# Kernel tuning notes

Measured on AMD Instinct MI355X. Metric: run time of the kernel, lower is better.

Reference implementation:

```python
import jax, jax.numpy as jnp
import numpy as np


def setup_inputs() -> dict:
    key = jax.random.key(0)
    ks = jax.random.split(key, 7)
    B, S, D, F, E = 4, 2048, 1024, 4096, 8
    scale = 0.02
    return {
        "x": jax.random.normal(ks[0], (B, S, D), dtype=jnp.float32),
        "gate_w": jax.random.normal(ks[1], (D, E), dtype=jnp.float32) * scale,
        "gate_b": jnp.zeros((E,), dtype=jnp.float32),
        "w1": jax.random.normal(ks[2], (E, D, F), dtype=jnp.float32) * scale,
        "b1": jnp.zeros((E, F), dtype=jnp.float32),
        "w2": jax.random.normal(ks[3], (E, F, D), dtype=jnp.float32) * scale,
        "b2": jnp.zeros((E, D), dtype=jnp.float32),
        "top_k": 2,
    }


def reference(x, gate_w, gate_b, w1, b1, w2, b2, top_k):
    B, S, D = x.shape
    E = w1.shape[0]
    xf = x.reshape(-1, D)                      # [T, D], T = B*S
    T = xf.shape[0]

    # Router: top-k logits, softmax over the selected k (as in torch code)
    logits = xf @ gate_w + gate_b              # [T, E]
    rw, sel = jax.lax.top_k(logits, top_k)     # [T, k], [T, k]
    w = jax.nn.softmax(rw, axis=-1)            # [T, k]

    # Dense combine weights: combine[t, e] = sum_k w[t,k] * (sel[t,k]==e)
    combine = jnp.zeros((T, E), dtype=xf.dtype)
    combine = combine.at[jnp.arange(T)[:, None], sel].add(w)

    # Loop over small fixed expert count; each expert FFN on all tokens,
    # weighted by combine (zero for unrouted tokens). Dropout p honored as 0 (eval).
    out = jnp.zeros_like(xf)
    for e in range(E):
        h = jax.nn.gelu(xf @ w1[e] + b1[e], approximate=False)  # torch F.gelu = exact
        out = out + combine[:, e:e + 1] * (h @ w2[e] + b2[e])
    return out.reshape(B, S, D)
```

## Files before the change

kernel.cpp:

```cpp
#include <hip/hip_runtime.h>
#include <math.h>

#define T_TOK 8192
#define DDIM  1024
#define FDIM  4096
#define NEXP  8
#define MAXTILES 136

typedef __attribute__((ext_vector_type(8))) short short8;
typedef __attribute__((ext_vector_type(4))) float f32x4;
typedef unsigned short u16;
typedef unsigned int   u32;

typedef const __attribute__((address_space(1))) u32* gp_t;
typedef       __attribute__((address_space(3))) u32* lp_t;

__device__ __forceinline__ void gload16(const void* g, void* l) {
  __builtin_amdgcn_global_load_lds((gp_t)g, (lp_t)l, 16, 0, 0);
}

__device__ __forceinline__ u16 f2bf(float f) {
  u32 u = __float_as_uint(f);
  u = u + 0x7FFFu + ((u >> 16) & 1u);
  return (u16)(u >> 16);
}

__device__ __forceinline__ float gelu_exact(float v) {
  return 0.5f * v * (1.0f + erff(v * 0.70710678118654752440f));
}

__device__ __forceinline__ int xcd_swz(int orig, int nwg) {
  int xcd = orig & 7;
  int q = nwg >> 3, r = nwg & 7;
  int base = (xcd < r) ? xcd * (q + 1) : r * (q + 1) + (xcd - r) * q;
  return base + (orig >> 3);
}

__global__ __launch_bounds__(256) void router_kernel(
    const float* __restrict__ x, const float* __restrict__ gw,
    const float* __restrict__ gb, u16* __restrict__ xb,
    int* __restrict__ counts, int* __restrict__ sel, float* __restrict__ wts)
{
  const int t    = blockIdx.x * 4 + (threadIdx.x >> 6);
  const int lane = threadIdx.x & 63;
  const float* xr = x + (size_t)t * DDIM;
  u16* xbr = xb + (size_t)t * DDIM;
  float lg[NEXP];
  #pragma unroll
  for (int e = 0; e < NEXP; e++) lg[e] = 0.f;
  #pragma unroll
  for (int i = 0; i < 4; i++) {
    int d0 = i * 256 + lane * 4;
    float4 v = *(const float4*)(xr + d0);
    ushort4 o;
    o.x = f2bf(v.x); o.y = f2bf(v.y); o.z = f2bf(v.z); o.w = f2bf(v.w);
    *(ushort4*)(xbr + d0) = o;
    const float* g = gw + (size_t)d0 * NEXP;
    #pragma unroll
    for (int e = 0; e < NEXP; e++)
      lg[e] += v.x * g[e] + v.y * g[NEXP + e] + v.z * g[2 * NEXP + e] + v.w * g[3 * NEXP + e];
  }
  #pragma unroll
  for (int off = 32; off > 0; off >>= 1) {
    #pragma unroll
    for (int e = 0; e < NEXP; e++) lg[e] += __shfl_down(lg[e], off);
  }
  if (lane == 0) {
    float v0 = -1e30f, v1 = -1e30f; int s0 = 0, s1 = 0;
    #pragma unroll
    for (int e = 0; e < NEXP; e++) {
      float v = lg[e] + gb[e];
      if (v > v0) { v1 = v0; s1 = s0; v0 = v; s0 = e; }
      else if (v > v1) { v1 = v; s1 = e; }
    }
    float a  = expf(v1 - v0);
    float w0 = 1.f / (1.f + a);
    sel[t * 2] = s0; sel[t * 2 + 1] = s1;
    wts[t * 2] = w0; wts[t * 2 + 1] = 1.f - w0;
    atomicAdd(&counts[s0], 1); atomicAdd(&counts[s1], 1);
  }
}

__global__ void scan_kernel(const int* __restrict__ counts,
                            int* __restrict__ offsets, int* __restrict__ pos,
                            int* __restrict__ map_e, int* __restrict__ map_r,
                            int* __restrict__ nT)
{
  if (threadIdx.x == 0) {
    int run = 0, nt = 0;
    for (int e = 0; e < NEXP; e++) {
      offsets[e] = run; pos[e] = run;
      int c = counts[e];
      int ntile = (c + 127) >> 7;
      for (int i = 0; i < ntile; i++) { map_e[nt] = e; map_r[nt] = i * 128; nt++; }
      run += c;
    }
    nT[0] = nt;
  }
}

__global__ __launch_bounds__(256) void slot_assign_kernel(
    const int* __restrict__ sel, const float* __restrict__ wts,
    int* __restrict__ pos, int* __restrict__ slot_token,
    float* __restrict__ slot_weight, int* __restrict__ token_slot)
{
  const int t = blockIdx.x * 256 + threadIdx.x;
  #pragma unroll
  for (int k = 0; k < 2; k++) {
    int e = sel[t * 2 + k];
    int p = atomicAdd(&pos[e], 1);
    slot_token[p] = t; slot_weight[p] = wts[t * 2 + k];
    token_slot[t * 2 + k] = p;
  }
}

__global__ __launch_bounds__(256) void wtrans_kernel(
    const float* __restrict__ in, u16* __restrict__ out, int M, int N)
{
  const int e = blockIdx.z;
  in  += (size_t)e * M * N;
  out += (size_t)e * M * N;
  const int c0 = blockIdx.x * 64;
  const int r0 = blockIdx.y * 64;
  __shared__ float tile[64][65];
  const int tid = threadIdx.x;
  const int tr = tid >> 4;
  const int tc = (tid & 15) * 4;
  #pragma unroll
  for (int p = 0; p < 4; p++) {
    int r = p * 16 + tr;
    float4 v = *(const float4*)(in + (size_t)(r0 + r) * N + (c0 + tc));
    tile[r][tc] = v.x; tile[r][tc + 1] = v.y; tile[r][tc + 2] = v.z; tile[r][tc + 3] = v.w;
  }
  __syncthreads();
  #pragma unroll
  for (int p = 0; p < 4; p++) {
    int oc = p * 16 + tr;
    ushort4 o;
    o.x = f2bf(tile[tc][oc]);     o.y = f2bf(tile[tc + 1][oc]);
    o.z = f2bf(tile[tc + 2][oc]); o.w = f2bf(tile[tc + 3][oc]);
    *(ushort4*)(out + (size_t)(c0 + oc) * M + (r0 + tc)) = o;
  }
}

__global__ __launch_bounds__(256) void gemm1_kernel(
    const u16* __restrict__ XB, const u16* __restrict__ W1T,
    const float* __restrict__ B1,
    const int* __restrict__ counts, const int* __restrict__ offsets,
    const int* __restrict__ slot_token,
    const int* __restrict__ map_e, const int* __restrict__ map_r,
    const int* __restrict__ nT, u16* __restrict__ H)
{
  const int gid   = xcd_swz(blockIdx.x, gridDim.x);
  const int n_idx = gid / MAXTILES;
  const int t_idx = gid - n_idx * MAXTILES;
  if (t_idx >= nT[0]) return;
  const int e    = map_e[t_idx];
  const int row0 = map_r[t_idx];
  const int cnt  = counts[e];
  const int off  = offsets[e];
  const int n0   = n_idx * 128;

  __shared__ __align__(16) u16 As[128 * 32];
  __shared__ __align__(16) u16 Bs[128 * 32];

  const int tid = threadIdx.x, wave = tid >> 6, lane = tid & 63;
  const int ca = wave * 64 + lane;
  const int rA0 = ca >> 2, sl0 = ca & 3;

  int t0 = slot_token[off + row0 + rA0];      if ((u32)t0 >= T_TOK) t0 = 0;
  int t1 = slot_token[off + row0 + rA0 + 64]; if ((u32)t1 >= T_TOK) t1 = 0;
  const char* gA0 = (const char*)XB + (((size_t)t0 * DDIM) + sl0 * 8) * 2;
  const char* gA1 = (const char*)XB + (((size_t)t1 * DDIM) + sl0 * 8) * 2;
  char* lA0 = (char*)As + wave * 1024;
  char* lA1 = (char*)As + 4096 + wave * 1024;

  const char* gB0 = (const char*)W1T + (((size_t)(e * FDIM + n0 + rA0)) * DDIM + sl0 * 8) * 2;
  const char* gB1 = (const char*)W1T + (((size_t)(e * FDIM + n0 + rA0 + 64)) * DDIM + sl0 * 8) * 2;
  char* lB0 = (char*)Bs + wave * 1024;
  char* lB1 = (char*)Bs + 4096 + wave * 1024;

  f32x4 acc[4][4] = {};
  const int wr = wave >> 1, wc = wave & 1;
  const int lr = lane & 15, lk = (lane >> 4) * 8;

  for (int k0 = 0; k0 < DDIM; k0 += 32) {
    __syncthreads();
    gload16(gA0 + k0 * 2, lA0);
    gload16(gA1 + k0 * 2, lA1);
    gload16(gB0 + k0 * 2, lB0);
    gload16(gB1 + k0 * 2, lB1);
    __syncthreads();

    short8 a[4], b[4];
    #pragma unroll
    for (int m = 0; m < 4; m++)
      a[m] = *(const short8*)&As[(wr * 64 + m * 16 + lr) * 32 + lk];
    #pragma unroll
    for (int n = 0; n < 4; n++)
      b[n] = *(const short8*)&Bs[(wc * 64 + n * 16 + lr) * 32 + lk];
    #pragma unroll
    for (int m = 0; m < 4; m++)
      #pragma unroll
      for (int n = 0; n < 4; n++)
        acc[m][n] = __builtin_amdgcn_mfma_f32_16x16x32_bf16(a[m], b[n], acc[m][n], 0, 0, 0);
  }

  #pragma unroll
  for (int nn = 0; nn < 4; nn++) {
    int col = n0 + wc * 64 + nn * 16 + lr;
    float b1v = B1[e * FDIM + col];
    #pragma unroll
    for (int m = 0; m < 4; m++) {
      int rbase = wr * 64 + m * 16 + (lane >> 4) * 4;
      #pragma unroll
      for (int j = 0; j < 4; j++) {
        int r = rbase + j;
        if (row0 + r < cnt) {
          float v = acc[m][nn][j] + b1v;
          H[(size_t)(off + row0 + r) * FDIM + col] = f2bf(gelu_exact(v));
        }
      }
    }
  }
}

__global__ __launch_bounds__(256) void gemm2_kernel(
    const u16* __restrict__ H, const u16* __restrict__ W2T,
    const float* __restrict__ B2,
    const int* __restrict__ counts, const int* __restrict__ offsets,
    const int* __restrict__ map_e, const int* __restrict__ map_r,
    const int* __restrict__ nT, float* __restrict__ Y)
{
  const int gid   = xcd_swz(blockIdx.x, gridDim.x);
  const int n_idx = gid / MAXTILES;
  const int t_idx = gid - n_idx * MAXTILES;
  if (t_idx >= nT[0]) return;
  const int e    = map_e[t_idx];
  const int row0 = map_r[t_idx];
  const int cnt  = counts[e];
  const int off  = offsets[e];
  const int n0   = n_idx * 128;

  __shared__ __align__(16) u16 As[128 * 32];
  __shared__ __align__(16) u16 Bs[128 * 32];

  const int tid = threadIdx.x, wave = tid >> 6, lane = tid & 63;
  const int ca = wave * 64 + lane;
  const int rA0 = ca >> 2, sl0 = ca & 3;

  const char* gA0 = (const char*)H + ((size_t)(off + row0 + rA0) * FDIM + sl0 * 8) * 2;
  const char* gA1 = (const char*)H + ((size_t)(off + row0 + rA0 + 64) * FDIM + sl0 * 8) * 2;
  char* lA0 = (char*)As + wave * 1024;
  char* lA1 = (char*)As + 4096 + wave * 1024;

  const char* gB0 = (const char*)W2T + ((size_t)(e * DDIM + n0 + rA0) * FDIM + sl0 * 8) * 2;
  const char* gB1 = (const char*)W2T + ((size_t)(e * DDIM + n0 + rA0 + 64) * FDIM + sl0 * 8) * 2;
  char* lB0 = (char*)Bs + wave * 1024;
  char* lB1 = (char*)Bs + 4096 + wave * 1024;

  f32x4 acc[4][4] = {};
  const int wr = wave >> 1, wc = wave & 1;
  const int lr = lane & 15, lk = (lane >> 4) * 8;

  for (int k0 = 0; k0 < FDIM; k0 += 32) {
    __syncthreads();
    gload16(gA0 + k0 * 2, lA0);
    gload16(gA1 + k0 * 2, lA1);
    gload16(gB0 + k0 * 2, lB0);
    gload16(gB1 + k0 * 2, lB1);
    __syncthreads();

    short8 a[4], b[4];
    #pragma unroll
    for (int m = 0; m < 4; m++)
      a[m] = *(const short8*)&As[(wr * 64 + m * 16 + lr) * 32 + lk];
    #pragma unroll
    for (int n = 0; n < 4; n++)
      b[n] = *(const short8*)&Bs[(wc * 64 + n * 16 + lr) * 32 + lk];
    #pragma unroll
    for (int m = 0; m < 4; m++)
      #pragma unroll
      for (int n = 0; n < 4; n++)
        acc[m][n] = __builtin_amdgcn_mfma_f32_16x16x32_bf16(a[m], b[n], acc[m][n], 0, 0, 0);
  }

  #pragma unroll
  for (int m = 0; m < 4; m++) {
    int rbase = wr * 64 + m * 16 + (lane >> 4) * 4;
    #pragma unroll
    for (int j = 0; j < 4; j++) {
      int r = rbase + j;
      if (row0 + r >= cnt) continue;
      size_t s = (size_t)(off + row0 + r);
      #pragma unroll
      for (int nn = 0; nn < 4; nn++) {
        int col = n0 + wc * 64 + nn * 16 + lr;
        Y[s * DDIM + col] = acc[m][nn][j] + B2[e * DDIM + col];
      }
    }
  }
}

__global__ __launch_bounds__(256) void combine_kernel(
    const float* __restrict__ Y, const int* __restrict__ token_slot,
    const float* __restrict__ wts, float* __restrict__ out)
{
  size_t gid = (size_t)blockIdx.x * 256 + threadIdx.x;
  int t = (int)(gid >> 8);
  int c = (int)(gid & 255) * 4;
  int s0 = token_slot[t * 2], s1 = token_slot[t * 2 + 1];
  float w0 = wts[t * 2], w1 = wts[t * 2 + 1];
  float4 y0 = *(const float4*)&Y[(size_t)s0 * DDIM + c];
  float4 y1 = *(const float4*)&Y[(size_t)s1 * DDIM + c];
  float4 o;
  o.x = w0 * y0.x + w1 * y1.x; o.y = w0 * y0.y + w1 * y1.y;
  o.z = w0 * y0.z + w1 * y1.z; o.w = w0 * y0.w + w1 * y1.w;
  *(float4*)&out[(size_t)t * DDIM + c] = o;
}

extern "C" void kernel_launch(void* const* d_in, const int* in_sizes, int n_in,
                              void* d_out, int out_size, void* d_ws, size_t ws_size,
                              hipStream_t stream)
{
  (void)in_sizes; (void)n_in; (void)out_size; (void)ws_size;
  const float* x  = (const float*)d_in[0];
  const float* gw = (const float*)d_in[1];
  const float* gb = (const float*)d_in[2];
  const float* w1 = (const float*)d_in[3];
  const float* b1 = (const float*)d_in[4];
  const float* w2 = (const float*)d_in[5];
  const float* b2 = (const float*)d_in[6];

  char* ws = (char*)d_ws;
  int*   counts = (int*)(ws + 0);
  int*   posp   = (int*)(ws + 64);
  int*   offp   = (int*)(ws + 128);
  int*   nT     = (int*)(ws + 192);
  int*   map_e  = (int*)(ws + 256);
  int*   map_r  = (int*)(ws + 1024);

  size_t p = 2048;
  int*   sel   = (int*)(ws + p);   p += (size_t)T_TOK * 2 * 4;
  float* wts   = (float*)(ws + p); p += (size_t)T_TOK * 2 * 4;
  int*   stok  = (int*)(ws + p);  p += (size_t)(2 * T_TOK + 256) * 4;
  float* swgt  = (float*)(ws + p); p += (size_t)(2 * T_TOK + 256) * 4;
  int*   tslot = (int*)(ws + p);  p += (size_t)T_TOK * 2 * 4;
  p = (p + 1048575) & ~(size_t)1048575;
  u16*   xb    = (u16*)(ws + p);  p += (size_t)T_TOK * DDIM * 2;
  u16*   w1t   = (u16*)(ws + p);  p += (size_t)NEXP * DDIM * FDIM * 2;
  u16*   w2t   = (u16*)(ws + p);  p += (size_t)NEXP * DDIM * FDIM * 2;
  u16*   Hbuf  = (u16*)(ws + p);  p += (size_t)(2 * T_TOK + 128) * FDIM * 2;
  float* Ybuf  = (float*)(ws + p);

  hipMemsetAsync(ws, 0, 256, stream);
  router_kernel<<<T_TOK / 4, 256, 0, stream>>>(x, gw, gb, xb, counts, sel, wts);
  scan_kernel<<<1, 64, 0, stream>>>(counts, offp, posp, map_e, map_r, nT);
  slot_assign_kernel<<<T_TOK / 256, 256, 0, stream>>>(sel, wts, posp, stok, swgt, tslot);
  wtrans_kernel<<<dim3(FDIM / 64, DDIM / 64, NEXP), 256, 0, stream>>>(w1, w1t, DDIM, FDIM);
  wtrans_kernel<<<dim3(DDIM / 64, FDIM / 64, NEXP), 256, 0, stream>>>(w2, w2t, FDIM, DDIM);

  gemm1_kernel<<<(FDIM / 128) * MAXTILES, 256, 0, stream>>>(
      xb, w1t, b1, counts, offp, stok, map_e, map_r, nT, Hbuf);
  gemm2_kernel<<<(DDIM / 128) * MAXTILES, 256, 0, stream>>>(
      Hbuf, w2t, b2, counts, offp, map_e, map_r, nT, Ybuf);

  combine_kernel<<<(T_TOK * DDIM / 4) / 256, 256, 0, stream>>>(Ybuf, tslot, wts, (float*)d_out);
}
```

Baseline: 923.0 us.

## Double-buffer GEMM LDS tiles, fuse combine via atomics, widen weight transpose

Both expert GEMMs now double-buffer their LDS tiles, so the next K-slice's global-to-LDS load is issued before the MFMAs on the current slice, with one barrier per iteration instead of two. The combine kernel and the Y buffer are removed: gemm2 scales its output by the routing weight and atomically adds it into a zeroed output, saving a full fp32 intermediate write and re-read. The weight transpose uses 128-row tiles and writes 16-byte bf16 vectors. In exchange, the atomics make the fp32 summation order non-deterministic, and the larger LDS footprint may lower occupancy.

```diff
diff --git a/kernel.cpp b/kernel.cpp
--- a/kernel.cpp
+++ b/kernel.cpp
@@ -102,7 +102,7 @@
 __global__ __launch_bounds__(256) void slot_assign_kernel(
     const int* __restrict__ sel, const float* __restrict__ wts,
     int* __restrict__ pos, int* __restrict__ slot_token,
-    float* __restrict__ slot_weight, int* __restrict__ token_slot)
+    float* __restrict__ slot_weight)
 {
   const int t = blockIdx.x * 256 + threadIdx.x;
   #pragma unroll
@@ -110,7 +110,6 @@
     int e = sel[t * 2 + k];
     int p = atomicAdd(&pos[e], 1);
     slot_token[p] = t; slot_weight[p] = wts[t * 2 + k];
-    token_slot[t * 2 + k] = p;
   }
 }
 
@@ -120,26 +119,28 @@
   const int e = blockIdx.z;
   in  += (size_t)e * M * N;
   out += (size_t)e * M * N;
+  const int r0 = blockIdx.y * 128;
   const int c0 = blockIdx.x * 64;
-  const int r0 = blockIdx.y * 64;
-  __shared__ float tile[64][65];
+  __shared__ float tile[128][65];
   const int tid = threadIdx.x;
-  const int tr = tid >> 4;
-  const int tc = (tid & 15) * 4;
+  const int lr = tid >> 4;
+  const int lc = (tid & 15) * 4;
+  #pragma unroll
+  for (int p = 0; p < 8; p++) {
+    int r = p * 16 + lr;
+    float4 v = *(const float4*)(in + (size_t)(r0 + r) * N + (c0 + lc));
+    tile[r][lc] = v.x; tile[r][lc + 1] = v.y; tile[r][lc + 2] = v.z; tile[r][lc + 3] = v.w;
+  }
+  __syncthreads();
+  const int oc = tid >> 4;
+  const int om = (tid & 15) * 8;
   #pragma unroll
   for (int p = 0; p < 4; p++) {
-    int r = p * 16 + tr;
-    float4 v = *(const float4*)(in + (size_t)(r0 + r) * N + (c0 + tc));
-    tile[r][tc] = v.x; tile[r][tc + 1] = v.y; tile[r][tc + 2] = v.z; tile[r][tc + 3] = v.w;
-  }
-  __syncthreads();
-  #pragma unroll
-  for (int p = 0; p < 4; p++) {
-    int oc = p * 16 + tr;
-    ushort4 o;
-    o.x = f2bf(tile[tc][oc]);     o.y = f2bf(tile[tc + 1][oc]);
-    o.z = f2bf(tile[tc + 2][oc]); o.w = f2bf(tile[tc + 3][oc]);
-    *(ushort4*)(out + (size_t)(c0 + oc) * M + (r0 + tc)) = o;
+    int c = p * 16 + oc;
+    short8 o;
+    #pragma unroll
+    for (int j = 0; j < 8; j++) o[j] = (short)f2bf(tile[om + j][c]);
+    *(short8*)(out + (size_t)(c0 + c) * M + (r0 + om)) = o;
   }
 }
 
@@ -161,8 +162,8 @@
   const int off  = offsets[e];
   const int n0   = n_idx * 128;
 
-  __shared__ __align__(16) u16 As[128 * 32];
-  __shared__ __align__(16) u16 Bs[128 * 32];
+  __shared__ __align__(16) u16 As[2][128 * 32];
+  __shared__ __align__(16) u16 Bs[2][128 * 32];
 
   const int tid = threadIdx.x, wave = tid >> 6, lane = tid & 63;
   const int ca = wave * 64 + lane;
@@ -172,38 +173,45 @@
   int t1 = slot_token[off + row0 + rA0 + 64]; if ((u32)t1 >= T_TOK) t1 = 0;
   const char* gA0 = (const char*)XB + (((size_t)t0 * DDIM) + sl0 * 8) * 2;
   const char* gA1 = (const char*)XB + (((size_t)t1 * DDIM) + sl0 * 8) * 2;
-  char* lA0 = (char*)As + wave * 1024;
-  char* lA1 = (char*)As + 4096 + wave * 1024;
-
   const char* gB0 = (const char*)W1T + (((size_t)(e * FDIM + n0 + rA0)) * DDIM + sl0 * 8) * 2;
   const char* gB1 = (const char*)W1T + (((size_t)(e * FDIM + n0 + rA0 + 64)) * DDIM + sl0 * 8) * 2;
-  char* lB0 = (char*)Bs + wave * 1024;
-  char* lB1 = (char*)Bs + 4096 + wave * 1024;
+
+  char* baseA = (char*)As;
+  char* baseB = (char*)Bs;
+  auto stage = [&](int buf, int k0) {
+    char* a = baseA + buf * 8192 + wave * 1024;
+    char* b = baseB + buf * 8192 + wave * 1024;
+    gload16(gA0 + (size_t)k0 * 2, a);
+    gload16(gA1 + (size_t)k0 * 2, a + 4096);
+    gload16(gB0 + (size_t)k0 * 2, b);
+    gload16(gB1 + (size_t)k0 * 2, b + 4096);
+  };
 
   f32x4 acc[4][4] = {};
   const int wr = wave >> 1, wc = wave & 1;
   const int lr = lane & 15, lk = (lane >> 4) * 8;
 
-  for (int k0 = 0; k0 < DDIM; k0 += 32) {
-    __syncthreads();
-    gload16(gA0 + k0 * 2, lA0);
-    gload16(gA1 + k0 * 2, lA1);
-    gload16(gB0 + k0 * 2, lB0);
-    gload16(gB1 + k0 * 2, lB1);
-    __syncthreads();
-
+  stage(0, 0);
+  __syncthreads();
+  int cur = 0;
+  for (int t = 0; t < DDIM / 32; t++) {
+    if (t + 1 < DDIM / 32) stage(cur ^ 1, (t + 1) * 32);
+    const u16* Ab = As[cur];
+    const u16* Bb = Bs[cur];
     short8 a[4], b[4];
     #pragma unroll
     for (int m = 0; m < 4; m++)
-      a[m] = *(const short8*)&As[(wr * 64 + m * 16 + lr) * 32 + lk];
+      a[m] = *(const short8*)&Ab[(wr * 64 + m * 16 + lr) * 32 + lk];
     #pragma unroll
     for (int n = 0; n < 4; n++)
-      b[n] = *(const short8*)&Bs[(wc * 64 + n * 16 + lr) * 32 + lk];
+      b[n] = *(const short8*)&Bb[(wc * 64 + n * 16 + lr) * 32 + lk];
     #pragma unroll
     for (int m = 0; m < 4; m++)
       #pragma unroll
       for (int n = 0; n < 4; n++)
         acc[m][n] = __builtin_amdgcn_mfma_f32_16x16x32_bf16(a[m], b[n], acc[m][n], 0, 0, 0);
+    __syncthreads();
+    cur ^= 1;
   }
 
   #pragma unroll
@@ -229,8 +237,9 @@
     const u16* __restrict__ H, const u16* __restrict__ W2T,
     const float* __restrict__ B2,
     const int* __restrict__ counts, const int* __restrict__ offsets,
+    const int* __restrict__ slot_token, const float* __restrict__ slot_weight,
     const int* __restrict__ map_e, const int* __restrict__ map_r,
-    const int* __restrict__ nT, float* __restrict__ Y)
+    const int* __restrict__ nT, float* __restrict__ out)
 {
   const int gid   = xcd_swz(blockIdx.x, gridDim.x);
   const int n_idx = gid / MAXTILES;
@@ -242,8 +251,8 @@
   const int off  = offsets[e];
   const int n0   = n_idx * 128;
 
-  __shared__ __align__(16) u16 As[128 * 32];
-  __shared__ __align__(16) u16 Bs[128 * 32];
+  __shared__ __align__(16) u16 As[2][128 * 32];
+  __shared__ __align__(16) u16 Bs[2][128 * 32];
 
   const int tid = threadIdx.x, wave = tid >> 6, lane = tid & 63;
   const int ca = wave * 64 + lane;
@@ -251,38 +260,45 @@
 
   const char* gA0 = (const char*)H + ((size_t)(off + row0 + rA0) * FDIM + sl0 * 8) * 2;
   const char* gA1 = (const char*)H + ((size_t)(off + row0 + rA0 + 64) * FDIM + sl0 * 8) * 2;
-  char* lA0 = (char*)As + wave * 1024;
-  char* lA1 = (char*)As + 4096 + wave * 1024;
-
   const char* gB0 = (const char*)W2T + ((size_t)(e * DDIM + n0 + rA0) * FDIM + sl0 * 8) * 2;
   const char* gB1 = (const char*)W2T + ((size_t)(e * DDIM + n0 + rA0 + 64) * FDIM + sl0 * 8) * 2;
-  char* lB0 = (char*)Bs + wave * 1024;
-  char* lB1 = (char*)Bs + 4096 + wave * 1024;
+
+  char* baseA = (char*)As;
+  char* baseB = (char*)Bs;
+  auto stage = [&](int buf, int k0) {
+    char* a = baseA + buf * 8192 + wave * 1024;
+    char* b = baseB + buf * 8192 + wave * 1024;
+    gload16(gA0 + (size_t)k0 * 2, a);
+    gload16(gA1 + (size_t)k0 * 2, a + 4096);
+    gload16(gB0 + (size_t)k0 * 2, b);
+    gload16(gB1 + (size_t)k0 * 2, b + 4096);
+  };
 
   f32x4 acc[4][4] = {};
   const int wr = wave >> 1, wc = wave & 1;
   const int lr = lane & 15, lk = (lane >> 4) * 8;
 
-  for (int k0 = 0; k0 < FDIM; k0 += 32) {
-    __syncthreads();
-    gload16(gA0 + k0 * 2, lA0);
-    gload16(gA1 + k0 * 2, lA1);
-    gload16(gB0 + k0 * 2, lB0);
-    gload16(gB1 + k0 * 2, lB1);
-    __syncthreads();
-
+  stage(0, 0);
+  __syncthreads();
+  int cur = 0;
+  for (int t = 0; t < FDIM / 32; t++) {
+    if (t + 1 < FDIM / 32) stage(cur ^ 1, (t + 1) * 32);
+    const u16* Ab = As[cur];
+    const u16* Bb = Bs[cur];
     short8 a[4], b[4];
     #pragma unroll
     for (int m = 0; m < 4; m++)
-      a[m] = *(const short8*)&As[(wr * 64 + m * 16 + lr) * 32 + lk];
+      a[m] = *(const short8*)&Ab[(wr * 64 + m * 16 + lr) * 32 + lk];
     #pragma unroll
     for (int n = 0; n < 4; n++)
-      b[n] = *(const short8*)&Bs[(wc * 64 + n * 16 + lr) * 32 + lk];
+      b[n] = *(const short8*)&Bb[(wc * 64 + n * 16 + lr) * 32 + lk];
     #pragma unroll
     for (int m = 0; m < 4; m++)
       #pragma unroll
       for (int n = 0; n < 4; n++)
         acc[m][n] = __builtin_amdgcn_mfma_f32_16x16x32_bf16(a[m], b[n], acc[m][n], 0, 0, 0);
+    __syncthreads();
+    cur ^= 1;
   }
 
   #pragma unroll
@@ -293,37 +309,23 @@
       int r = rbase + j;
       if (row0 + r >= cnt) continue;
       size_t s = (size_t)(off + row0 + r);
+      int tok = slot_token[s];
+      float wgt = slot_weight[s];
       #pragma unroll
       for (int nn = 0; nn < 4; nn++) {
         int col = n0 + wc * 64 + nn * 16 + lr;
-        Y[s * DDIM + col] = acc[m][nn][j] + B2[e * DDIM + col];
+        float v = (acc[m][nn][j] + B2[e * DDIM + col]) * wgt;
+        atomicAdd(&out[(size_t)tok * DDIM + col], v);
       }
     }
   }
-}
-
-__global__ __launch_bounds__(256) void combine_kernel(
-    const float* __restrict__ Y, const int* __restrict__ token_slot,
-    const float* __restrict__ wts, float* __restrict__ out)
-{
-  size_t gid = (size_t)blockIdx.x * 256 + threadIdx.x;
-  int t = (int)(gid >> 8);
-  int c = (int)(gid & 255) * 4;
-  int s0 = token_slot[t * 2], s1 = token_slot[t * 2 + 1];
-  float w0 = wts[t * 2], w1 = wts[t * 2 + 1];
-  float4 y0 = *(const float4*)&Y[(size_t)s0 * DDIM + c];
-  float4 y1 = *(const float4*)&Y[(size_t)s1 * DDIM + c];
-  float4 o;
-  o.x = w0 * y0.x + w1 * y1.x; o.y = w0 * y0.y + w1 * y1.y;
-  o.z = w0 * y0.z + w1 * y1.z; o.w = w0 * y0.w + w1 * y1.w;
-  *(float4*)&out[(size_t)t * DDIM + c] = o;
 }
 
 extern "C" void kernel_launch(void* const* d_in, const int* in_sizes, int n_in,
                               void* d_out, int out_size, void* d_ws, size_t ws_size,
                               hipStream_t stream)
 {
-  (void)in_sizes; (void)n_in; (void)out_size; (void)ws_size;
+  (void)in_sizes; (void)n_in; (void)ws_size;
   const float* x  = (const float*)d_in[0];
   const float* gw = (const float*)d_in[1];
   const float* gb = (const float*)d_in[2];
@@ -343,27 +345,24 @@
   size_t p = 2048;
   int*   sel   = (int*)(ws + p);   p += (size_t)T_TOK * 2 * 4;
   float* wts   = (float*)(ws + p); p += (size_t)T_TOK * 2 * 4;
-  int*   stok  = (int*)(ws + p);  p += (size_t)(2 * T_TOK + 256) * 4;
+  int*   stok  = (int*)(ws + p);   p += (size_t)(2 * T_TOK + 256) * 4;
   float* swgt  = (float*)(ws + p); p += (size_t)(2 * T_TOK + 256) * 4;
-  int*   tslot = (int*)(ws + p);  p += (size_t)T_TOK * 2 * 4;
   p = (p + 1048575) & ~(size_t)1048575;
-  u16*   xb    = (u16*)(ws + p);  p += (size_t)T_TOK * DDIM * 2;
-  u16*   w1t   = (u16*)(ws + p);  p += (size_t)NEXP * DDIM * FDIM * 2;
-  u16*   w2t   = (u16*)(ws + p);  p += (size_t)NEXP * DDIM * FDIM * 2;
-  u16*   Hbuf  = (u16*)(ws + p);  p += (size_t)(2 * T_TOK + 128) * FDIM * 2;
-  float* Ybuf  = (float*)(ws + p);
+  u16*   xb    = (u16*)(ws + p);   p += (size_t)T_TOK * DDIM * 2;
+  u16*   w1t   = (u16*)(ws + p);   p += (size_t)NEXP * DDIM * FDIM * 2;
+  u16*   w2t   = (u16*)(ws + p);   p += (size_t)NEXP * DDIM * FDIM * 2;
+  u16*   Hbuf  = (u16*)(ws + p);
 
   hipMemsetAsync(ws, 0, 256, stream);
+  hipMemsetAsync(d_out, 0, (size_t)out_size * sizeof(float), stream);
   router_kernel<<<T_TOK / 4, 256, 0, stream>>>(x, gw, gb, xb, counts, sel, wts);
   scan_kernel<<<1, 64, 0, stream>>>(counts, offp, posp, map_e, map_r, nT);
-  slot_assign_kernel<<<T_TOK / 256, 256, 0, stream>>>(sel, wts, posp, stok, swgt, tslot);
-  wtrans_kernel<<<dim3(FDIM / 64, DDIM / 64, NEXP), 256, 0, stream>>>(w1, w1t, DDIM, FDIM);
-  wtrans_kernel<<<dim3(DDIM / 64, FDIM / 64, NEXP), 256, 0, stream>>>(w2, w2t, FDIM, DDIM);
+  slot_assign_kernel<<<T_TOK / 256, 256, 0, stream>>>(sel, wts, posp, stok, swgt);
+  wtrans_kernel<<<dim3(DDIM / 64, FDIM / 128, NEXP), 256, 0, stream>>>(w2, w2t, FDIM, DDIM);
+  wtrans_kernel<<<dim3(FDIM / 64, DDIM / 128, NEXP), 256, 0, stream>>>(w1, w1t, DDIM, FDIM);
 
   gemm1_kernel<<<(FDIM / 128) * MAXTILES, 256, 0, stream>>>(
       xb, w1t, b1, counts, offp, stok, map_e, map_r, nT, Hbuf);
   gemm2_kernel<<<(DDIM / 128) * MAXTILES, 256, 0, stream>>>(
-      Hbuf, w2t, b2, counts, offp, map_e, map_r, nT, Ybuf);
-
-  combine_kernel<<<(T_TOK * DDIM / 4) / 256, 256, 0, stream>>>(Ybuf, tslot, wts, (float*)d_out);
-}
+      Hbuf, w2t, b2, counts, offp, stok, swgt, map_e, map_r, nT, (float*)d_out);
+}
```

After: 971.6 us. 5.3% more time.
